# Optimization experiments

Hardware: AMD Instinct MI355X
Metric: run time of the kernel (lower is better)

Reference implementation:

```python
import jax, jax.numpy as jnp
import numpy as np

B, N, H = 8, 256, 768
P = 128          # path_hidden_size
HEADS = 12
D = H // HEADS   # 64
EPS = 1e-5


def layer_norm(x, g, b):
    mu = jnp.mean(x, axis=-1, keepdims=True)
    var = jnp.mean((x - mu) ** 2, axis=-1, keepdims=True)
    return (x - mu) * jax.lax.rsqrt(var + EPS) * g + b


def setup_inputs() -> dict:
    key = jax.random.key(0)
    ks = jax.random.split(key, 16)
    s = 0.02
    return {
        "nodes": jax.random.normal(ks[0], (B, N, H), jnp.float32),
        "bias": jax.random.normal(ks[1], (B, HEADS, N, N), jnp.float32),
        "paths": jax.random.normal(ks[2], (B, N, N, P), jnp.float32),
        "Wq": jax.random.normal(ks[3], (H, H), jnp.float32) * s,
        "bq": jnp.zeros((H,), jnp.float32),
        "Wk": jax.random.normal(ks[4], (H, H), jnp.float32) * s,
        "bk": jnp.zeros((H,), jnp.float32),
        "Wv": jax.random.normal(ks[5], (H, H), jnp.float32) * s,
        "bv": jnp.zeros((H,), jnp.float32),
        "Wsk": jax.random.normal(ks[6], (P, D), jnp.float32) * s,
        "bsk": jnp.zeros((D,), jnp.float32),
        "Wsv": jax.random.normal(ks[7], (P, D), jnp.float32) * s,
        "bsv": jnp.zeros((D,), jnp.float32),
        "Wo": jax.random.normal(ks[8], (H, H), jnp.float32) * s,
        "bo": jnp.zeros((H,), jnp.float32),
        "g_path": jnp.ones((P,), jnp.float32),
        "b_path": jnp.zeros((P,), jnp.float32),
        "g_out": jnp.ones((H,), jnp.float32),
        "b_out": jnp.zeros((H,), jnp.float32),
    }


def reference(nodes, bias, paths, Wq, bq, Wk, bk, Wv, bv, Wsk, bsk, Wsv, bsv,
              Wo, bo, g_path, b_path, g_out, b_out):
    # q/k/v: [B,N,H] -> [B,heads,N,D]
    def split(x):
        return x.reshape(B, N, HEADS, D).transpose(0, 2, 1, 3)

    q = split(nodes @ Wq + bq)
    k = split(nodes @ Wk + bk)
    v = split(nodes @ Wv + bv)

    pn = layer_norm(paths, g_path, b_path)          # [B,N,N,P]
    struct_k = pn @ Wsk + bsk                       # [B,N,N,D]
    struct_v = pn @ Wsv + bsv                       # [B,N,N,D]

    q = q * (D ** -0.5)
    # content scores + per-query-row structural scores + bias
    w = (jnp.einsum('bhqd,bhkd->bhqk', q, k)
         + jnp.einsum('bhqd,bqkd->bhqk', q, struct_k)
         + bias)
    w = jax.nn.softmax(w, axis=-1)                  # [B,heads,N,N]

    out = (jnp.einsum('bhqk,bhkd->bhqd', w, v)
           + jnp.einsum('bhqk,bqkd->bhqd', w, struct_v))
    out = out.transpose(0, 2, 1, 3).reshape(B, N, H)  # combine heads
    out = jax.nn.relu(out @ Wo + bo)
    # dropout is identity in eval mode
    return layer_norm(nodes + out, g_out, b_out)
```

## Files before the change

kernel.cpp:

```cpp
#include <hip/hip_runtime.h>
#include <stdint.h>

#define Bb 8
#define Nn 256
#define Hh 768
#define Pp 128
#define HEADS 12
#define Dd 64
#define EPSf 1e-5f

typedef __attribute__((ext_vector_type(8))) short bhalf8;
typedef __attribute__((ext_vector_type(4))) float f32x4;

__device__ __forceinline__ unsigned short f2bf(float f) {
    union { float f; unsigned u; } v; v.f = f;
    unsigned r = v.u + 0x7FFFu + ((v.u >> 16) & 1u);
    return (unsigned short)(r >> 16);
}

__device__ __forceinline__ int swz(int row, int colUs) {
    return colUs ^ ((row & 7) << 3);
}

__global__ __launch_bounds__(256) void k_transpose4(const float* __restrict__ a0, const float* __restrict__ a1,
                                                    const float* __restrict__ a2, const float* __restrict__ a3,
                                                    unsigned short* __restrict__ o0, unsigned short* __restrict__ o1,
                                                    unsigned short* __restrict__ o2, unsigned short* __restrict__ o3) {
    __shared__ float tile[32][33];
    int z = blockIdx.z;
    const float* in = (z == 0) ? a0 : (z == 1) ? a1 : (z == 2) ? a2 : a3;
    unsigned short* out = (z == 0) ? o0 : (z == 1) ? o1 : (z == 2) ? o2 : o3;
    const int R = 768, C = 768;
    int c0 = blockIdx.x * 32, r0 = blockIdx.y * 32;
    int tx = threadIdx.x & 31, ty = threadIdx.x >> 5;
    for (int i = ty; i < 32; i += 8)
        tile[i][tx] = in[(size_t)(r0 + i) * C + c0 + tx];
    __syncthreads();
    for (int i = ty; i < 32; i += 8)
        out[(size_t)(c0 + i) * R + r0 + tx] = f2bf(tile[tx][i]);
}

__global__ __launch_bounds__(256) void k_transpose_small(const float* __restrict__ a0, const float* __restrict__ a1,
                                                         const float* __restrict__ gp,
                                                         unsigned short* __restrict__ o0, unsigned short* __restrict__ o1) {
    __shared__ float tile[32][33];
    int z = blockIdx.z;
    const float* in = (z == 0) ? a0 : a1;
    unsigned short* out = (z == 0) ? o0 : o1;
    const int R = 128, C = 64;
    int c0 = blockIdx.x * 32, r0 = blockIdx.y * 32;
    int tx = threadIdx.x & 31, ty = threadIdx.x >> 5;
    for (int i = ty; i < 32; i += 8)
        tile[i][tx] = in[(size_t)(r0 + i) * C + c0 + tx];
    __syncthreads();
    float g = gp[r0 + tx];
    for (int i = ty; i < 32; i += 8)
        out[(size_t)(c0 + i) * R + r0 + tx] = f2bf(tile[tx][i] * g);
}

__global__ __launch_bounds__(128) void k_prep_bias(const float* __restrict__ Wsk, const float* __restrict__ Wsv,
                                                   const float* __restrict__ bp,
                                                   const float* __restrict__ bsk, const float* __restrict__ bsv,
                                                   float* __restrict__ bskv2) {
    int d = threadIdx.x;
    const float* W = (d < 64) ? Wsk : Wsv;
    int dd = d & 63;
    float s = (d < 64) ? bsk[dd] : bsv[dd];
    for (int p2 = 0; p2 < 128; p2++) s += bp[p2] * W[p2 * 64 + dd];
    bskv2[d] = s;
}

__global__ __launch_bounds__(256) void k_qkv(const float* __restrict__ nodes,
                                             const unsigned short* __restrict__ Wt,
                                             const float* __restrict__ bq, const float* __restrict__ bk,
                                             const float* __restrict__ bv,
                                             float* __restrict__ qs, float* __restrict__ kk,
                                             unsigned short* __restrict__ vt) {
    __shared__ __align__(16) unsigned short Alds[64 * 72];
    __shared__ __align__(16) unsigned short Blds[128 * 72];
    int tid = threadIdx.x;
    int m0 = blockIdx.y * 64;
    int n0 = blockIdx.x * 128;
    int w = tid >> 6, lane = tid & 63;
    int wm = w >> 1, wn = w & 1;
    int lm = lane & 15, lq = lane >> 4;
    f32x4 acc[2][4];
#pragma unroll
    for (int i = 0; i < 2; i++)
#pragma unroll
        for (int j = 0; j < 4; j++) acc[i][j] = (f32x4){0.f, 0.f, 0.f, 0.f};

    for (int kt = 0; kt < 768; kt += 64) {
#pragma unroll
        for (int t = 0; t < 4; t++) {
            int c = t * 256 + tid;
            int row = c >> 4, cc = c & 15;
            float4 v = *(const float4*)(nodes + (size_t)(m0 + row) * 768 + kt + cc * 4);
            uint2 uu;
            uu.x = (unsigned)f2bf(v.x) | ((unsigned)f2bf(v.y) << 16);
            uu.y = (unsigned)f2bf(v.z) | ((unsigned)f2bf(v.w) << 16);
            *(uint2*)(Alds + row * 72 + cc * 4) = uu;
        }
#pragma unroll
        for (int t = 0; t < 4; t++) {
            int c = t * 256 + tid;
            int n = c >> 3, kc = c & 7;
            uint4 v = *(const uint4*)(Wt + (size_t)(n0 + n) * 768 + kt + kc * 8);
            *(uint4*)(Blds + n * 72 + kc * 8) = v;
        }
        __syncthreads();
#pragma unroll
        for (int ks = 0; ks < 2; ks++) {
            bhalf8 af[2];
#pragma unroll
            for (int mi = 0; mi < 2; mi++)
                af[mi] = *(const bhalf8*)(Alds + (wm * 32 + mi * 16 + lm) * 72 + ks * 32 + lq * 8);
#pragma unroll
            for (int nt = 0; nt < 4; nt++) {
                bhalf8 bf = *(const bhalf8*)(Blds + (wn * 64 + nt * 16 + lm) * 72 + ks * 32 + lq * 8);
#pragma unroll
                for (int mi = 0; mi < 2; mi++)
                    acc[mi][nt] = __builtin_amdgcn_mfma_f32_16x16x32_bf16(af[mi], bf, acc[mi][nt], 0, 0, 0);
            }
        }
        __syncthreads();
    }
    int wsel = n0 / 768;
    int nb = n0 % 768;
    if (wsel == 2) {
#pragma unroll
        for (int mi = 0; mi < 2; mi++)
#pragma unroll
            for (int nt = 0; nt < 4; nt++)
#pragma unroll
                for (int r = 0; r < 4; r++) {
                    int row = m0 + wm * 32 + mi * 16 + lq * 4 + r;
                    int col = nb + wn * 64 + nt * 16 + lm;
                    int hh = col >> 6, d = col & 63;
                    int b = row >> 8, qn = row & 255;
                    float val = acc[mi][nt][r] + bv[col];
                    vt[(((size_t)b * HEADS + hh) * Dd + d) * Nn + qn] = f2bf(val);
                }
    } else {
        const float* bias = (wsel == 0) ? bq : bk;
        float* dst = (wsel == 0) ? qs : kk;
        float scale = (wsel == 0) ? 0.125f : 1.0f;
#pragma unroll
        for (int mi = 0; mi < 2; mi++)
#pragma unroll
            for (int nt = 0; nt < 4; nt++)
#pragma unroll
                for (int r = 0; r < 4; r++) {
                    int row = m0 + wm * 32 + mi * 16 + lq * 4 + r;
                    int col = nb + wn * 64 + nt * 16 + lm;
                    int hh = col >> 6, d = col & 63;
                    int b = row >> 8, qn = row & 255;
                    float val = (acc[mi][nt][r] + bias[col]) * scale;
                    dst[(((size_t)b * HEADS + hh) * Nn + qn) * Dd + d] = val;
                }
    }
}

__global__ __launch_bounds__(256) void k_scores(const float* __restrict__ qs,
                                                const float* __restrict__ kk,
                                                const float* __restrict__ bias,
                                                float* __restrict__ wg) {
    __shared__ __align__(16) unsigned short Alds[64 * 72];
    __shared__ __align__(16) unsigned short Blds[64 * 72];
    int tid = threadIdx.x;
    int bh = blockIdx.z;
    int m0 = blockIdx.y * 64;
    int n0 = blockIdx.x * 64;
    int w = tid >> 6, lane = tid & 63, lm = lane & 15, lq = lane >> 4;
    const float* Abase = qs + ((size_t)bh * Nn + m0) * Dd;
    const float* Bbase = kk + ((size_t)bh * Nn + n0) * Dd;
#pragma unroll
    for (int t = 0; t < 4; t++) {
        int c = t * 256 + tid;
        int row = c >> 4, cc = c & 15;
        float4 va = *(const float4*)(Abase + (size_t)row * 64 + cc * 4);
        uint2 ua;
        ua.x = (unsigned)f2bf(va.x) | ((unsigned)f2bf(va.y) << 16);
        ua.y = (unsigned)f2bf(va.z) | ((unsigned)f2bf(va.w) << 16);
        *(uint2*)(Alds + row * 72 + cc * 4) = ua;
        float4 vb = *(const float4*)(Bbase + (size_t)row * 64 + cc * 4);
        uint2 ub;
        ub.x = (unsigned)f2bf(vb.x) | ((unsigned)f2bf(vb.y) << 16);
        ub.y = (unsigned)f2bf(vb.z) | ((unsigned)f2bf(vb.w) << 16);
        *(uint2*)(Blds + row * 72 + cc * 4) = ub;
    }
    __syncthreads();
    f32x4 acc[4];
#pragma unroll
    for (int i = 0; i < 4; i++) acc[i] = (f32x4){0.f, 0.f, 0.f, 0.f};
#pragma unroll
    for (int ks = 0; ks < 2; ks++) {
        bhalf8 af = *(const bhalf8*)(Alds + (w * 16 + lm) * 72 + ks * 32 + lq * 8);
#pragma unroll
        for (int nt = 0; nt < 4; nt++) {
            bhalf8 bf = *(const bhalf8*)(Blds + (nt * 16 + lm) * 72 + ks * 32 + lq * 8);
            acc[nt] = __builtin_amdgcn_mfma_f32_16x16x32_bf16(af, bf, acc[nt], 0, 0, 0);
        }
    }
#pragma unroll
    for (int nt = 0; nt < 4; nt++)
#pragma unroll
        for (int r = 0; r < 4; r++) {
            int row = m0 + w * 16 + lq * 4 + r;
            int col = n0 + nt * 16 + lm;
            size_t idx = ((size_t)bh * Nn + row) * Nn + col;
            wg[idx] = acc[nt][r] + bias[idx];
        }
}

__global__ __launch_bounds__(512, 4) void k_attn(const float* __restrict__ qs,
                                                 const float* __restrict__ paths,
                                                 const unsigned short* __restrict__ Wskvt,
                                                 const float* __restrict__ bskv2,
                                                 const float* __restrict__ wg,
                                                 unsigned short* __restrict__ wgbf,
                                                 float* __restrict__ attn) {
    __shared__ __align__(16) unsigned short SKbuf[256 * 64];
    __shared__ __align__(16) unsigned short A2buf[16 * 256];
    unsigned short* SVT = SKbuf;
    float* redm = (float*)A2buf;
    float* reds = ((float*)A2buf) + 128;

    int tid = threadIdx.x;
    int bq = blockIdx.x;
    int b = bq >> 8, q = bq & 255;
    int w = tid >> 6, lane = tid & 63, lm = lane & 15, lq = lane >> 4;

    const float* ppath = paths + (size_t)bq * (256 * 128);

    bhalf8 afr[2][4];
#pragma unroll
    for (int mi = 0; mi < 2; mi++) {
        int R = w * 32 + mi * 16 + lm;
        const float* pr = ppath + (size_t)R * 128;
        float x[32];
#pragma unroll
        for (int ks = 0; ks < 4; ks++) {
            float4 a = *(const float4*)(pr + ks * 32 + lq * 8);
            float4 c = *(const float4*)(pr + ks * 32 + lq * 8 + 4);
            x[ks * 8 + 0] = a.x; x[ks * 8 + 1] = a.y; x[ks * 8 + 2] = a.z; x[ks * 8 + 3] = a.w;
            x[ks * 8 + 4] = c.x; x[ks * 8 + 5] = c.y; x[ks * 8 + 6] = c.z; x[ks * 8 + 7] = c.w;
        }
        float s = 0.f, s2 = 0.f;
#pragma unroll
        for (int i = 0; i < 32; i++) { s += x[i]; s2 += x[i] * x[i]; }
        s  += __shfl_xor(s, 16);  s2 += __shfl_xor(s2, 16);
        s  += __shfl_xor(s, 32);  s2 += __shfl_xor(s2, 32);
        float mu = s * (1.f / 128.f);
        float var = s2 * (1.f / 128.f) - mu * mu;
        float rs = rsqrtf(var + EPSf);
#pragma unroll
        for (int ks = 0; ks < 4; ks++) {
            bhalf8 t;
#pragma unroll
            for (int j = 0; j < 8; j++)
                t[j] = (short)f2bf((x[ks * 8 + j] - mu) * rs);
            afr[mi][ks] = t;
        }
    }

    {
        f32x4 acc[2][4];
#pragma unroll
        for (int i = 0; i < 2; i++)
#pragma unroll
            for (int j = 0; j < 4; j++) acc[i][j] = (f32x4){0.f, 0.f, 0.f, 0.f};
#pragma unroll
        for (int ks = 0; ks < 4; ks++) {
#pragma unroll
            for (int nt = 0; nt < 4; nt++) {
                bhalf8 bf = *(const bhalf8*)(Wskvt + (size_t)(nt * 16 + lm) * 128 + ks * 32 + lq * 8);
#pragma unroll
                for (int mi = 0; mi < 2; mi++)
                    acc[mi][nt] = __builtin_amdgcn_mfma_f32_16x16x32_bf16(afr[mi][ks], bf, acc[mi][nt], 0, 0, 0);
            }
        }
#pragma unroll
        for (int mi = 0; mi < 2; mi++)
#pragma unroll
            for (int nt = 0; nt < 4; nt++) {
                int col = nt * 16 + lm;
                float bb = bskv2[col];
#pragma unroll
                for (int rr = 0; rr < 4; rr++) {
                    int R2 = w * 32 + mi * 16 + lq * 4 + rr;
                    SKbuf[R2 * 64 + swz(R2, col)] = f2bf(acc[mi][nt][rr] + bb);
                }
            }
    }

    f32x4 accSV[2][4];
#pragma unroll
    for (int i = 0; i < 2; i++)
#pragma unroll
        for (int j = 0; j < 4; j++) accSV[i][j] = (f32x4){0.f, 0.f, 0.f, 0.f};
#pragma unroll
    for (int ks = 0; ks < 4; ks++) {
#pragma unroll
        for (int nt = 0; nt < 4; nt++) {
            bhalf8 bf = *(const bhalf8*)(Wskvt + (size_t)(64 + nt * 16 + lm) * 128 + ks * 32 + lq * 8);
#pragma unroll
            for (int mi = 0; mi < 2; mi++)
                accSV[mi][nt] = __builtin_amdgcn_mfma_f32_16x16x32_bf16(afr[mi][ks], bf, accSV[mi][nt], 0, 0, 0);
        }
    }


    bhalf8 af1[2];
    {
        bhalf8 z = (bhalf8){0, 0, 0, 0, 0, 0, 0, 0};
        af1[0] = z; af1[1] = z;
        if (lm < 12) {
            const float* qp = qs + (((size_t)b * HEADS + lm) * Nn + q) * Dd;
#pragma unroll
            for (int ks = 0; ks < 2; ks++) {
                float4 v0 = *(const float4*)(qp + ks * 32 + lq * 8);
                float4 v1 = *(const float4*)(qp + ks * 32 + lq * 8 + 4);
                bhalf8 t;
                t[0] = (short)f2bf(v0.x); t[1] = (short)f2bf(v0.y);
                t[2] = (short)f2bf(v0.z); t[3] = (short)f2bf(v0.w);
                t[4] = (short)f2bf(v1.x); t[5] = (short)f2bf(v1.y);
                t[6] = (short)f2bf(v1.z); t[7] = (short)f2bf(v1.w);
                af1[ks] = t;
            }
        }
    }

    size_t wbase = ((size_t)b * HEADS) * (Nn * Nn) + (size_t)q * Nn;
    float wgv[2][4];
#pragma unroll
    for (int nt = 0; nt < 2; nt++) {
        int col = w * 32 + nt * 16 + lm;
#pragma unroll
        for (int r = 0; r < 4; r++) {
            int row = lq * 4 + r;
            wgv[nt][r] = (row < 12) ? wg[wbase + (size_t)row * (Nn * Nn) + col] : 0.f;
        }
    }

    f32x4 acc1[2];
#pragma unroll
    for (int i = 0; i < 2; i++) acc1[i] = (f32x4){0.f, 0.f, 0.f, 0.f};
#pragma unroll
    for (int ks = 0; ks < 2; ks++) {
#pragma unroll
        for (int nt = 0; nt < 2; nt++) {
            int row = w * 32 + nt * 16 + lm;
            bhalf8 bf = *(const bhalf8*)(SKbuf + row * 64 + swz(row, ks * 32 + lq * 8));
            acc1[nt] = __builtin_amdgcn_mfma_f32_16x16x32_bf16(af1[ks], bf, acc1[nt], 0, 0, 0);
        }
    }
    float S[2][4];
#pragma unroll
    for (int nt = 0; nt < 2; nt++)
#pragma unroll
        for (int r = 0; r < 4; r++) S[nt][r] = acc1[nt][r] + wgv[nt][r];

    __syncthreads();
#pragma unroll
    for (int mi = 0; mi < 2; mi++)
#pragma unroll
        for (int nt = 0; nt < 4; nt++) {
            int d = nt * 16 + lm;
            float bb = bskv2[64 + d];
#pragma unroll
            for (int rr = 0; rr < 4; rr++) {
                int R2 = w * 32 + mi * 16 + lq * 4 + rr;
                SVT[d * 256 + swz(d, R2)] = f2bf(accSV[mi][nt][rr] + bb);
            }
        }

    float m4[4];
#pragma unroll
    for (int r = 0; r < 4; r++)
        m4[r] = fmaxf(S[0][r], S[1][r]);
#pragma unroll
    for (int mk = 1; mk < 16; mk <<= 1)
#pragma unroll
        for (int r = 0; r < 4; r++) m4[r] = fmaxf(m4[r], __shfl_xor(m4[r], mk));
    if (lm == 0) {
#pragma unroll
        for (int r = 0; r < 4; r++) redm[(lq * 4 + r) * 8 + w] = m4[r];
    }
    __syncthreads();
    float rowmax[4];
#pragma unroll
    for (int r = 0; r < 4; r++) {
        int row = lq * 4 + r;
        float a = fmaxf(fmaxf(redm[row * 8 + 0], redm[row * 8 + 1]), fmaxf(redm[row * 8 + 2], redm[row * 8 + 3]));
        float c = fmaxf(fmaxf(redm[row * 8 + 4], redm[row * 8 + 5]), fmaxf(redm[row * 8 + 6], redm[row * 8 + 7]));
        rowmax[r] = fmaxf(a, c);
    }
    float P[2][4], psum[4];
#pragma unroll
    for (int r = 0; r < 4; r++) {
#pragma unroll
        for (int nt = 0; nt < 2; nt++) P[nt][r] = __expf(S[nt][r] - rowmax[r]);
        psum[r] = P[0][r] + P[1][r];
    }
#pragma unroll
    for (int mk = 1; mk < 16; mk <<= 1)
#pragma unroll
        for (int r = 0; r < 4; r++) psum[r] += __shfl_xor(psum[r], mk);
    if (lm == 0) {
#pragma unroll
        for (int r = 0; r < 4; r++) reds[(lq * 4 + r) * 8 + w] = psum[r];
    }
    __syncthreads();
    float inv[4];
#pragma unroll
    for (int r = 0; r < 4; r++) {
        int row = lq * 4 + r;
        float a = (reds[row * 8 + 0] + reds[row * 8 + 1]) + (reds[row * 8 + 2] + reds[row * 8 + 3]);
        float c = (reds[row * 8 + 4] + reds[row * 8 + 5]) + (reds[row * 8 + 6] + reds[row * 8 + 7]);
        inv[r] = 1.f / (a + c);
    }
    __syncthreads();
#pragma unroll
    for (int nt = 0; nt < 2; nt++)
#pragma unroll
        for (int r = 0; r < 4; r++) {
            int row = lq * 4 + r;
            int col = w * 32 + nt * 16 + lm;
            float pv = P[nt][r] * inv[r];
            unsigned short pb = f2bf(pv);
            A2buf[row * 256 + swz(row, col)] = pb;
            if (row < 12) wgbf[wbase + (size_t)row * (Nn * Nn) + col] = pb;
        }
    __syncthreads();

    if (w < 4) {
        f32x4 acc2 = (f32x4){0.f, 0.f, 0.f, 0.f};
#pragma unroll
        for (int ks = 0; ks < 8; ks++) {
            bhalf8 af = *(const bhalf8*)(A2buf + lm * 256 + swz(lm, ks * 32 + lq * 8));
            int vrow = w * 16 + lm;
            bhalf8 bf = *(const bhalf8*)(SVT + vrow * 256 + swz(vrow, ks * 32 + lq * 8));
            acc2 = __builtin_amdgcn_mfma_f32_16x16x32_bf16(af, bf, acc2, 0, 0, 0);
        }
#pragma unroll
        for (int r = 0; r < 4; r++) {
            int row = lq * 4 + r;
            if (row < 12) attn[(size_t)bq * Hh + row * 64 + w * 16 + lm] = acc2[r];
        }
    }
}

__global__ __launch_bounds__(256) void k_ctxout(const unsigned short* __restrict__ wgbf,
                                                const unsigned short* __restrict__ vt,
                                                float* __restrict__ attn) {
    __shared__ __align__(16) unsigned short Alds[64 * 72];
    __shared__ __align__(16) unsigned short Blds[64 * 72];
    int tid = threadIdx.x;
    int bh = blockIdx.y;
    int m0 = blockIdx.x * 64;
    int b = bh / 12, h = bh % 12;
    int w = tid >> 6, lane = tid & 63, lm = lane & 15, lq = lane >> 4;
    f32x4 acc[4];
#pragma unroll
    for (int i = 0; i < 4; i++) acc[i] = (f32x4){0.f, 0.f, 0.f, 0.f};
    const unsigned short* Abase = wgbf + ((size_t)bh * Nn + m0) * Nn;
    const unsigned short* Bbase = vt + (size_t)bh * Dd * Nn;
    for (int kt = 0; kt < 256; kt += 64) {
#pragma unroll
        for (int t = 0; t < 2; t++) {
            int c = t * 256 + tid;
            int row = c >> 3, kc = c & 7;
            *(uint4*)(Alds + row * 72 + kc * 8) = *(const uint4*)(Abase + (size_t)row * Nn + kt + kc * 8);
            *(uint4*)(Blds + row * 72 + kc * 8) = *(const uint4*)(Bbase + (size_t)row * Nn + kt + kc * 8);
        }
        __syncthreads();
#pragma unroll
        for (int ks = 0; ks < 2; ks++) {
            bhalf8 af = *(const bhalf8*)(Alds + (w * 16 + lm) * 72 + ks * 32 + lq * 8);
#pragma unroll
            for (int nt = 0; nt < 4; nt++) {
                bhalf8 bf = *(const bhalf8*)(Blds + (nt * 16 + lm) * 72 + ks * 32 + lq * 8);
                acc[nt] = __builtin_amdgcn_mfma_f32_16x16x32_bf16(af, bf, acc[nt], 0, 0, 0);
            }
        }
        __syncthreads();
    }
#pragma unroll
    for (int nt = 0; nt < 4; nt++)
#pragma unroll
        for (int r = 0; r < 4; r++) {
            int row = m0 + w * 16 + lq * 4 + r;
            int col = nt * 16 + lm;
            size_t o = ((size_t)b * Nn + row) * Hh + h * 64 + col;
            attn[o] += acc[nt][r];
        }
}

__global__ __launch_bounds__(256) void k_outproj(const float* __restrict__ attn,
                                                 const unsigned short* __restrict__ Wot,
                                                 const float* __restrict__ bo,
                                                 const float* __restrict__ nodes,
                                                 float* __restrict__ tmp) {
    __shared__ __align__(16) unsigned short Alds[64 * 72];
    __shared__ __align__(16) unsigned short Blds[128 * 72];
    int tid = threadIdx.x;
    int m0 = blockIdx.y * 64;
    int n0 = blockIdx.x * 128;
    int w = tid >> 6, lane = tid & 63;
    int wm = w >> 1, wn = w & 1;
    int lm = lane & 15, lq = lane >> 4;
    f32x4 acc[2][4];
#pragma unroll
    for (int i = 0; i < 2; i++)
#pragma unroll
        for (int j = 0; j < 4; j++) acc[i][j] = (f32x4){0.f, 0.f, 0.f, 0.f};
    for (int kt = 0; kt < 768; kt += 64) {
#pragma unroll
        for (int t = 0; t < 4; t++) {
            int c = t * 256 + tid;
            int row = c >> 4, cc = c & 15;
            float4 v = *(const float4*)(attn + (size_t)(m0 + row) * 768 + kt + cc * 4);
            uint2 uu;
            uu.x = (unsigned)f2bf(v.x) | ((unsigned)f2bf(v.y) << 16);
            uu.y = (unsigned)f2bf(v.z) | ((unsigned)f2bf(v.w) << 16);
            *(uint2*)(Alds + row * 72 + cc * 4) = uu;
        }
#pragma unroll
        for (int t = 0; t < 4; t++) {
            int c = t * 256 + tid;
            int n = c >> 3, kc = c & 7;
            uint4 v = *(const uint4*)(Wot + (size_t)(n0 + n) * 768 + kt + kc * 8);
            *(uint4*)(Blds + n * 72 + kc * 8) = v;
        }
        __syncthreads();
#pragma unroll
        for (int ks = 0; ks < 2; ks++) {
            bhalf8 af[2];
#pragma unroll
            for (int mi = 0; mi < 2; mi++)
                af[mi] = *(const bhalf8*)(Alds + (wm * 32 + mi * 16 + lm) * 72 + ks * 32 + lq * 8);
#pragma unroll
            for (int nt = 0; nt < 4; nt++) {
                bhalf8 bf = *(const bhalf8*)(Blds + (wn * 64 + nt * 16 + lm) * 72 + ks * 32 + lq * 8);
#pragma unroll
                for (int mi = 0; mi < 2; mi++)
                    acc[mi][nt] = __builtin_amdgcn_mfma_f32_16x16x32_bf16(af[mi], bf, acc[mi][nt], 0, 0, 0);
            }
        }
        __syncthreads();
    }
#pragma unroll
    for (int mi = 0; mi < 2; mi++)
#pragma unroll
        for (int nt = 0; nt < 4; nt++)
#pragma unroll
            for (int r = 0; r < 4; r++) {
                int row = m0 + wm * 32 + mi * 16 + lq * 4 + r;
                int col = n0 + wn * 64 + nt * 16 + lm;
                float val = acc[mi][nt][r] + bo[col];
                val = fmaxf(val, 0.f) + nodes[(size_t)row * 768 + col];
                tmp[(size_t)row * 768 + col] = val;
            }
}

__global__ __launch_bounds__(256) void k_finalln(const float* __restrict__ tmp,
                                                 const float* __restrict__ go,
                                                 const float* __restrict__ bout,
                                                 float* __restrict__ out) {
    __shared__ float rs1[4], rs2[4];
    int m = blockIdx.x, tid = threadIdx.x;
    int lane = tid & 63, wid = tid >> 6;
    const float* row = tmp + (size_t)m * 768;
    float x0 = row[tid], x1 = row[tid + 256], x2 = row[tid + 512];
    float s = x0 + x1 + x2;
    float s2 = x0 * x0 + x1 * x1 + x2 * x2;
#pragma unroll
    for (int mk = 32; mk; mk >>= 1) {
        s += __shfl_xor(s, mk);
        s2 += __shfl_xor(s2, mk);
    }
    if (lane == 0) { rs1[wid] = s; rs2[wid] = s2; }
    __syncthreads();
    s = rs1[0] + rs1[1] + rs1[2] + rs1[3];
    s2 = rs2[0] + rs2[1] + rs2[2] + rs2[3];
    float mu = s * (1.f / 768.f);
    float var = s2 * (1.f / 768.f) - mu * mu;
    float rstd = rsqrtf(var + EPSf);
    float* orow = out + (size_t)m * 768;
    orow[tid] = (x0 - mu) * rstd * go[tid] + bout[tid];
    orow[tid + 256] = (x1 - mu) * rstd * go[tid + 256] + bout[tid + 256];
    orow[tid + 512] = (x2 - mu) * rstd * go[tid + 512] + bout[tid + 512];
}

extern "C" void kernel_launch(void* const* d_in, const int* in_sizes, int n_in,
                              void* d_out, int out_size, void* d_ws, size_t ws_size,
                              hipStream_t stream) {
    const float* nodes = (const float*)d_in[0];
    const float* bias  = (const float*)d_in[1];
    const float* paths = (const float*)d_in[2];
    const float* Wq = (const float*)d_in[3];  const float* bq  = (const float*)d_in[4];
    const float* Wk = (const float*)d_in[5];  const float* bk  = (const float*)d_in[6];
    const float* Wv = (const float*)d_in[7];  const float* bv  = (const float*)d_in[8];
    const float* Wsk = (const float*)d_in[9]; const float* bsk = (const float*)d_in[10];
    const float* Wsv = (const float*)d_in[11];const float* bsv = (const float*)d_in[12];
    const float* Wo = (const float*)d_in[13]; const float* bo  = (const float*)d_in[14];
    const float* gp = (const float*)d_in[15]; const float* bp  = (const float*)d_in[16];
    const float* go = (const float*)d_in[17]; const float* bout= (const float*)d_in[18];
    float* out = (float*)d_out;

    char* ws = (char*)d_ws;
    size_t off = 0;
    auto carve = [&](size_t bytes) -> char* {
        char* p = ws + off;
        off += (bytes + 255) & ~(size_t)255;
        return p;
    };
    float* qs   = (float*)carve((size_t)Bb * HEADS * Nn * Dd * 4);
    float* kk   = (float*)carve((size_t)Bb * HEADS * Nn * Dd * 4);
    unsigned short* vt = (unsigned short*)carve((size_t)Bb * HEADS * Dd * Nn * 2);
    float* wg   = (float*)carve((size_t)Bb * HEADS * Nn * Nn * 4);
    unsigned short* wgbf = (unsigned short*)carve((size_t)Bb * HEADS * Nn * Nn * 2);
    float* attn = (float*)carve((size_t)Bb * Nn * Hh * 4);
    float* tmp  = (float*)carve((size_t)Bb * Nn * Hh * 4);
    unsigned short* Wqkvt = (unsigned short*)carve((size_t)3 * 768 * 768 * 2);
    unsigned short* Wot   = (unsigned short*)carve((size_t)768 * 768 * 2);
    unsigned short* Wskvt = (unsigned short*)carve((size_t)128 * 128 * 2);
    float* bskv2 = (float*)carve(128 * 4);
    (void)ws_size; (void)in_sizes; (void)n_in; (void)out_size;

    hipLaunchKernelGGL(k_transpose4, dim3(24, 24, 4), dim3(256), 0, stream,
                       Wq, Wk, Wv, Wo,
                       Wqkvt, Wqkvt + (size_t)768 * 768, Wqkvt + (size_t)2 * 768 * 768, Wot);
    hipLaunchKernelGGL(k_transpose_small, dim3(2, 4, 2), dim3(256), 0, stream,
                       Wsk, Wsv, gp, Wskvt, Wskvt + (size_t)64 * 128);
    hipLaunchKernelGGL(k_prep_bias, dim3(1), dim3(128), 0, stream,
                       Wsk, Wsv, bp, bsk, bsv, bskv2);

    hipLaunchKernelGGL(k_qkv, dim3(18, 32), dim3(256), 0, stream, nodes, Wqkvt, bq, bk, bv, qs, kk, vt);
    hipLaunchKernelGGL(k_scores, dim3(4, 4, 96), dim3(256), 0, stream, qs, kk, bias, wg);
    hipLaunchKernelGGL(k_attn, dim3(2048), dim3(512), 0, stream, qs, paths, Wskvt, bskv2, wg, wgbf, attn);
    hipLaunchKernelGGL(k_ctxout, dim3(4, 96), dim3(256), 0, stream, wgbf, vt, attn);
    hipLaunchKernelGGL(k_outproj, dim3(6, 32), dim3(256), 0, stream, attn, Wot, bo, nodes, tmp);
    hipLaunchKernelGGL(k_finalln, dim3(2048), dim3(256), 0, stream, tmp, go, bout, out);
}
```

Baseline: 558.6 us.

## Shrink k_attn LDS by splitting struct_v PV into two halves; smaller outproj tiles

In k_attn, the shared buffers are resized: the probability tile and only half of the transposed struct_v (32 of 64 dims) now share one buffer. The PV matmul runs in two passes with extra barriers, and one barrier before the A2 write is removed. This cuts LDS per block so more blocks can be resident on a CU, at the cost of added synchronisation and serialised PV work. Separately, k_outproj tiles go from 64x128 to 32x64, quadrupling the grid to fill more CUs, at the cost of less operand reuse per block.

After: 558.4 us. Within noise of the previous version (-0.0%).

```diff
diff --git a/kernel.cpp b/kernel.cpp
--- a/kernel.cpp
+++ b/kernel.cpp
@@ -220,11 +220,12 @@
                                                  const float* __restrict__ wg,
                                                  unsigned short* __restrict__ wgbf,
                                                  float* __restrict__ attn) {
-    __shared__ __align__(16) unsigned short SKbuf[256 * 64];
-    __shared__ __align__(16) unsigned short A2buf[16 * 256];
-    unsigned short* SVT = SKbuf;
-    float* redm = (float*)A2buf;
-    float* reds = ((float*)A2buf) + 128;
+    __shared__ __align__(16) unsigned short SH[256 * 64];
+    __shared__ float red[256];
+    unsigned short* A2 = SH;
+    unsigned short* SVTh = SH + 4096;
+    float* redm = red;
+    float* reds = red + 128;
 
     int tid = threadIdx.x;
     int bq = blockIdx.x;
@@ -289,7 +290,7 @@
 #pragma unroll
                 for (int rr = 0; rr < 4; rr++) {
                     int R2 = w * 32 + mi * 16 + lq * 4 + rr;
-                    SKbuf[R2 * 64 + swz(R2, col)] = f2bf(acc[mi][nt][rr] + bb);
+                    SH[R2 * 64 + swz(R2, col)] = f2bf(acc[mi][nt][rr] + bb);
                 }
             }
     }
@@ -351,7 +352,7 @@
 #pragma unroll
         for (int nt = 0; nt < 2; nt++) {
             int row = w * 32 + nt * 16 + lm;
-            bhalf8 bf = *(const bhalf8*)(SKbuf + row * 64 + swz(row, ks * 32 + lq * 8));
+            bhalf8 bf = *(const bhalf8*)(SH + row * 64 + swz(row, ks * 32 + lq * 8));
             acc1[nt] = __builtin_amdgcn_mfma_f32_16x16x32_bf16(af1[ks], bf, acc1[nt], 0, 0, 0);
         }
     }
@@ -362,16 +363,17 @@
         for (int r = 0; r < 4; r++) S[nt][r] = acc1[nt][r] + wgv[nt][r];
 
     __syncthreads();
+
 #pragma unroll
     for (int mi = 0; mi < 2; mi++)
 #pragma unroll
-        for (int nt = 0; nt < 4; nt++) {
+        for (int nt = 0; nt < 2; nt++) {
             int d = nt * 16 + lm;
             float bb = bskv2[64 + d];
 #pragma unroll
             for (int rr = 0; rr < 4; rr++) {
                 int R2 = w * 32 + mi * 16 + lq * 4 + rr;
-                SVT[d * 256 + swz(d, R2)] = f2bf(accSV[mi][nt][rr] + bb);
+                SVTh[d * 256 + swz(d, R2)] = f2bf(accSV[mi][nt][rr] + bb);
             }
         }
 
@@ -420,7 +422,6 @@
         float c = (reds[row * 8 + 4] + reds[row * 8 + 5]) + (reds[row * 8 + 6] + reds[row * 8 + 7]);
         inv[r] = 1.f / (a + c);
     }
-    __syncthreads();
 #pragma unroll
     for (int nt = 0; nt < 2; nt++)
 #pragma unroll
@@ -429,18 +430,50 @@
             int col = w * 32 + nt * 16 + lm;
             float pv = P[nt][r] * inv[r];
             unsigned short pb = f2bf(pv);
-            A2buf[row * 256 + swz(row, col)] = pb;
+            A2[row * 256 + swz(row, col)] = pb;
             if (row < 12) wgbf[wbase + (size_t)row * (Nn * Nn) + col] = pb;
         }
     __syncthreads();
 
-    if (w < 4) {
+    if (w < 2) {
         f32x4 acc2 = (f32x4){0.f, 0.f, 0.f, 0.f};
 #pragma unroll
         for (int ks = 0; ks < 8; ks++) {
-            bhalf8 af = *(const bhalf8*)(A2buf + lm * 256 + swz(lm, ks * 32 + lq * 8));
+            bhalf8 af = *(const bhalf8*)(A2 + lm * 256 + swz(lm, ks * 32 + lq * 8));
             int vrow = w * 16 + lm;
-            bhalf8 bf = *(const bhalf8*)(SVT + vrow * 256 + swz(vrow, ks * 32 + lq * 8));
+            bhalf8 bf = *(const bhalf8*)(SVTh + vrow * 256 + swz(vrow, ks * 32 + lq * 8));
+            acc2 = __builtin_amdgcn_mfma_f32_16x16x32_bf16(af, bf, acc2, 0, 0, 0);
+        }
+#pragma unroll
+        for (int r = 0; r < 4; r++) {
+            int row = lq * 4 + r;
+            if (row < 12) attn[(size_t)bq * Hh + row * 64 + w * 16 + lm] = acc2[r];
+        }
+    }
+    __syncthreads();
+
+#pragma unroll
+    for (int mi = 0; mi < 2; mi++)
+#pragma unroll
+        for (int nt = 2; nt < 4; nt++) {
+            int d = nt * 16 + lm;
+            int dr = d - 32;
+            float bb = bskv2[64 + d];
+#pragma unroll
+            for (int rr = 0; rr < 4; rr++) {
+                int R2 = w * 32 + mi * 16 + lq * 4 + rr;
+                SVTh[dr * 256 + swz(dr, R2)] = f2bf(accSV[mi][nt][rr] + bb);
+            }
+        }
+    __syncthreads();
+
+    if (w >= 2 && w < 4) {
+        f32x4 acc2 = (f32x4){0.f, 0.f, 0.f, 0.f};
+#pragma unroll
+        for (int ks = 0; ks < 8; ks++) {
+            bhalf8 af = *(const bhalf8*)(A2 + lm * 256 + swz(lm, ks * 32 + lq * 8));
+            int vrow = (w - 2) * 16 + lm;
+            bhalf8 bf = *(const bhalf8*)(SVTh + vrow * 256 + swz(vrow, ks * 32 + lq * 8));
             acc2 = __builtin_amdgcn_mfma_f32_16x16x32_bf16(af, bf, acc2, 0, 0, 0);
         }
 #pragma unroll
@@ -502,22 +535,20 @@
                                                  const float* __restrict__ bo,
                                                  const float* __restrict__ nodes,
                                                  float* __restrict__ tmp) {
-    __shared__ __align__(16) unsigned short Alds[64 * 72];
-    __shared__ __align__(16) unsigned short Blds[128 * 72];
+    __shared__ __align__(16) unsigned short Alds[32 * 72];
+    __shared__ __align__(16) unsigned short Blds[64 * 72];
     int tid = threadIdx.x;
-    int m0 = blockIdx.y * 64;
-    int n0 = blockIdx.x * 128;
+    int m0 = blockIdx.y * 32;
+    int n0 = blockIdx.x * 64;
     int w = tid >> 6, lane = tid & 63;
     int wm = w >> 1, wn = w & 1;
     int lm = lane & 15, lq = lane >> 4;
-    f32x4 acc[2][4];
-#pragma unroll
-    for (int i = 0; i < 2; i++)
-#pragma unroll
-        for (int j = 0; j < 4; j++) acc[i][j] = (f32x4){0.f, 0.f, 0.f, 0.f};
+    f32x4 acc[2];
+#pragma unroll
+    for (int j = 0; j < 2; j++) acc[j] = (f32x4){0.f, 0.f, 0.f, 0.f};
     for (int kt = 0; kt < 768; kt += 64) {
 #pragma unroll
-        for (int t = 0; t < 4; t++) {
+        for (int t = 0; t < 2; t++) {
             int c = t * 256 + tid;
             int row = c >> 4, cc = c & 15;
             float4 v = *(const float4*)(attn + (size_t)(m0 + row) * 768 + kt + cc * 4);
@@ -527,7 +558,7 @@
             *(uint2*)(Alds + row * 72 + cc * 4) = uu;
         }
 #pragma unroll
-        for (int t = 0; t < 4; t++) {
+        for (int t = 0; t < 2; t++) {
             int c = t * 256 + tid;
             int n = c >> 3, kc = c & 7;
             uint4 v = *(const uint4*)(Wot + (size_t)(n0 + n) * 768 + kt + kc * 8);
@@ -536,32 +567,25 @@
         __syncthreads();
 #pragma unroll
         for (int ks = 0; ks < 2; ks++) {
-            bhalf8 af[2];
-#pragma unroll
-            for (int mi = 0; mi < 2; mi++)
-                af[mi] = *(const bhalf8*)(Alds + (wm * 32 + mi * 16 + lm) * 72 + ks * 32 + lq * 8);
-#pragma unroll
-            for (int nt = 0; nt < 4; nt++) {
-                bhalf8 bf = *(const bhalf8*)(Blds + (wn * 64 + nt * 16 + lm) * 72 + ks * 32 + lq * 8);
-#pragma unroll
-                for (int mi = 0; mi < 2; mi++)
-                    acc[mi][nt] = __builtin_amdgcn_mfma_f32_16x16x32_bf16(af[mi], bf, acc[mi][nt], 0, 0, 0);
+            bhalf8 af = *(const bhalf8*)(Alds + (wm * 16 + lm) * 72 + ks * 32 + lq * 8);
+#pragma unroll
+            for (int nt = 0; nt < 2; nt++) {
+                bhalf8 bf = *(const bhalf8*)(Blds + (wn * 32 + nt * 16 + lm) * 72 + ks * 32 + lq * 8);
+                acc[nt] = __builtin_amdgcn_mfma_f32_16x16x32_bf16(af, bf, acc[nt], 0, 0, 0);
             }
         }
         __syncthreads();
     }
 #pragma unroll
-    for (int mi = 0; mi < 2; mi++)
-#pragma unroll
-        for (int nt = 0; nt < 4; nt++)
-#pragma unroll
-            for (int r = 0; r < 4; r++) {
-                int row = m0 + wm * 32 + mi * 16 + lq * 4 + r;
-                int col = n0 + wn * 64 + nt * 16 + lm;
-                float val = acc[mi][nt][r] + bo[col];
-                val = fmaxf(val, 0.f) + nodes[(size_t)row * 768 + col];
-                tmp[(size_t)row * 768 + col] = val;
-            }
+    for (int nt = 0; nt < 2; nt++)
+#pragma unroll
+        for (int r = 0; r < 4; r++) {
+            int row = m0 + wm * 16 + lq * 4 + r;
+            int col = n0 + wn * 32 + nt * 16 + lm;
+            float val = acc[nt][r] + bo[col];
+            val = fmaxf(val, 0.f) + nodes[(size_t)row * 768 + col];
+            tmp[(size_t)row * 768 + col] = val;
+        }
 }
 
 __global__ __launch_bounds__(256) void k_finalln(const float* __restrict__ tmp,
@@ -641,6 +665,6 @@
     hipLaunchKernelGGL(k_scores, dim3(4, 4, 96), dim3(256), 0, stream, qs, kk, bias, wg);
     hipLaunchKernelGGL(k_attn, dim3(2048), dim3(512), 0, stream, qs, paths, Wskvt, bskv2, wg, wgbf, attn);
     hipLaunchKernelGGL(k_ctxout, dim3(4, 96), dim3(256), 0, stream, wgbf, vt, attn);
-    hipLaunchKernelGGL(k_outproj, dim3(6, 32), dim3(256), 0, stream, attn, Wot, bo, nodes, tmp);
+    hipLaunchKernelGGL(k_outproj, dim3(12, 64), dim3(256), 0, stream, attn, Wot, bo, nodes, tmp);
     hipLaunchKernelGGL(k_finalln, dim3(2048), dim3(256), 0, stream, tmp, go, bout, out);
 }
```
